# Performance work log

Hardware: AMD Instinct MI355X
Metric: run time of the kernel (lower is better)

## Reference

```python
import jax, jax.numpy as jnp
import numpy as np

EPS = 1e-8  # F.cosine_similarity default eps


def setup_inputs() -> dict:
    key = jax.random.key(0)
    k1, k2, k3 = jax.random.split(key, 3)
    C, S, Q, D_IN, Z_DIM = 256, 5, 64, 1024, 128
    xs = jax.random.normal(k1, (C, S, D_IN), dtype=jnp.float32)
    xq = jax.random.normal(k2, (C, Q, D_IN), dtype=jnp.float32)
    W = jax.random.normal(k3, (D_IN, Z_DIM), dtype=jnp.float32) / np.sqrt(D_IN)
    return {"xs": xs, "xq": xq, "W": W}


def _protonet_loss(xs, xq, W):
    C, S, D = xs.shape
    Q = xq.shape[1]
    # encoder (linear) applied to concatenated support+query, as in the original
    x = jnp.concatenate([xs.reshape(C * S, D), xq.reshape(C * Q, D)], axis=0)
    z = x @ W                                   # [C*(S+Q), Zd]
    Zd = z.shape[-1]
    z_proto = z[: C * S].reshape(C, S, Zd).mean(axis=1)   # [C, Zd]
    zq = z[C * S:]                                        # [C*Q, Zd]
    # squared euclidean distance (GEMM form, avoids [CQ, C, Zd] intermediate)
    d2 = (jnp.sum(zq * zq, axis=-1, keepdims=True)
          + jnp.sum(z_proto * z_proto, axis=-1)[None, :]
          - 2.0 * (zq @ z_proto.T))                       # [C*Q, C]
    lp = d2.reshape(C, Q, C)                              # label_predicts
    # leave-one-out: for each class i drop column i -> [C, Q, C-1]
    loo_idx = np.stack([np.delete(np.arange(C), i) for i in range(C)])  # [C, C-1]
    idx = jnp.broadcast_to(jnp.asarray(loo_idx)[:, None, :], (C, Q, C - 1))
    loo = jnp.take_along_axis(lp, idx, axis=2)            # [C, Q, C-1]
    # pairwise cosine similarity between query rows j<k, per class
    nrm = jnp.maximum(jnp.linalg.norm(loo, axis=-1), EPS)
    a = loo / nrm[..., None]
    sim = jnp.einsum('cqd,ckd->cqk', a, a)                # [C, Q, Q]
    pair_mask = jnp.triu(jnp.ones((Q, Q), dtype=bool), 1)
    n_pairs = C * (Q * (Q - 1) // 2)
    cos_loss = jnp.sum(jnp.where(pair_mask[None], sim, 0.0)) / n_pairs
    # log_softmax over prototype axis; accuracy vs diagonal targets
    log_p_y = jax.nn.log_softmax(-d2, axis=1).reshape(C, Q, C)
    y_hat = jnp.argmax(log_p_y, axis=2)                   # [C, Q]
    acc = jnp.mean((y_hat == jnp.arange(C)[:, None]).astype(jnp.float32))
    # original overwrites loss_val with the cosine-similarity loss
    return cos_loss, acc


def reference(xs, xq, W):
    return _protonet_loss(xs, xq, W)
```

## Files before the change

kernel.cpp:

```cpp
#include <hip/hip_runtime.h>


typedef __attribute__((ext_vector_type(8))) short s8v;
typedef __attribute__((ext_vector_type(4))) float f32x4;

__device__ __forceinline__ short f2bf(float f) {
  union { float f; unsigned u; } v; v.f = f;
  unsigned r = (v.u + 0x7fffu + ((v.u >> 16) & 1u)) >> 16;
  return (short)r;
}

__global__ void k_zero(float* __restrict__ out) {
  if (threadIdx.x < 2) out[threadIdx.x] = 0.0f;
}

__global__ void k_xbar(const float* __restrict__ xs, float* __restrict__ xbar) {
  const int c = blockIdx.x;
  const float* b = xs + (size_t)c * 5120;
  for (int e = threadIdx.x; e < 1024; e += 256) {
    float s = b[e] + b[1024 + e] + b[2048 + e] + b[3072 + e] + b[4096 + e];
    xbar[(size_t)c * 1024 + e] = s * 0.2f;
  }
}

__global__ __launch_bounds__(256) void k_wt(const float* __restrict__ W,
                                            unsigned short* __restrict__ Wt) {
  __shared__ unsigned short T[128 * 68];
  const int tid = threadIdx.x;
  const int kb = blockIdx.x * 64;
#pragma unroll
  for (int s = 0; s < 8; ++s) {
    int idx = tid + s * 256;
    int kr = idx >> 5, n4 = idx & 31;
    float4 v = *(const float4*)(W + (size_t)(kb + kr) * 128 + n4 * 4);
    T[(n4 * 4 + 0) * 68 + kr] = (unsigned short)f2bf(v.x);
    T[(n4 * 4 + 1) * 68 + kr] = (unsigned short)f2bf(v.y);
    T[(n4 * 4 + 2) * 68 + kr] = (unsigned short)f2bf(v.z);
    T[(n4 * 4 + 3) * 68 + kr] = (unsigned short)f2bf(v.w);
  }
  __syncthreads();
#pragma unroll
  for (int s = 0; s < 8; ++s) {
    int idx = tid + s * 256;
    int n = idx >> 4, k4 = idx & 15;
    ushort4 o;
    o.x = T[n * 68 + k4 * 4 + 0];
    o.y = T[n * 68 + k4 * 4 + 1];
    o.z = T[n * 68 + k4 * 4 + 2];
    o.w = T[n * 68 + k4 * 4 + 3];
    *(ushort4*)(Wt + (size_t)n * 1024 + kb + k4 * 4) = o;
  }
}

__global__ __launch_bounds__(64) void k_gemm_z(
    const float* __restrict__ xbar, const float* __restrict__ xq,
    const unsigned short* __restrict__ Wt,
    unsigned short* __restrict__ zb, float* __restrict__ n2) {
  const int rb = blockIdx.x * 16;
  const int lane = threadIdx.x & 63, ln = lane & 15, q = lane >> 4;
  const float* abase = (rb < 256) ? (xbar + (size_t)rb * 1024)
                                  : (xq + (size_t)(rb - 256) * 1024);
  const float* arow = abase + (size_t)ln * 1024 + q * 8;
  f32x4 acc[8] = {};
  float4 a0 = *(const float4*)(arow);
  float4 a1 = *(const float4*)(arow + 4);
  for (int kt = 0; kt < 32; ++kt) {
    float4 p0, p1;
    if (kt < 31) {
      p0 = *(const float4*)(arow + (kt + 1) * 32);
      p1 = *(const float4*)(arow + (kt + 1) * 32 + 4);
    }
    s8v af = { f2bf(a0.x), f2bf(a0.y), f2bf(a0.z), f2bf(a0.w),
               f2bf(a1.x), f2bf(a1.y), f2bf(a1.z), f2bf(a1.w) };
#pragma unroll
    for (int t = 0; t < 8; ++t) {
      s8v bf = *(const s8v*)(Wt + (size_t)(t * 16 + ln) * 1024 + kt * 32 + q * 8);
      acc[t] = __builtin_amdgcn_mfma_f32_16x16x32_bf16(af, bf, acc[t], 0, 0, 0);
    }
    a0 = p0; a1 = p1;
  }
#pragma unroll
  for (int p = 0; p < 4; ++p) {
    int grow = rb + q * 4 + p;
    float sp = 0.0f;
#pragma unroll
    for (int t = 0; t < 8; ++t) {
      float v = acc[t][p];
      zb[(size_t)grow * 128 + t * 16 + ln] = (unsigned short)f2bf(v);
      sp += v * v;
    }
    sp += __shfl_xor(sp, 1);
    sp += __shfl_xor(sp, 2);
    sp += __shfl_xor(sp, 4);
    sp += __shfl_xor(sp, 8);
    if (ln == 0) n2[grow] = sp;
  }
}

__global__ __launch_bounds__(256) void k_d2red(
    const unsigned short* __restrict__ zb, const float* __restrict__ n2,
    float* __restrict__ out) {
  __shared__ float Dt[256 * 65];
  __shared__ float rv[256];
  __shared__ int   ri[256];
  __shared__ float rss[256];
  __shared__ float invn[64];
  __shared__ float sred[4];
  __shared__ float s_tc, s_aq2, s_corr;
  const int tid = threadIdx.x;
  const int c = blockIdx.x;
  const int w = tid >> 6, lane = tid & 63, ln = lane & 15, qd = lane >> 4;

  f32x4 acc[16] = {};
  const unsigned short* Az = zb + (size_t)(256 + c * 64 + w * 16 + ln) * 128;
#pragma unroll
  for (int kt = 0; kt < 4; ++kt) {
    s8v af = *(const s8v*)(Az + kt * 32 + qd * 8);
#pragma unroll
    for (int t = 0; t < 16; ++t) {
      s8v bf = *(const s8v*)(zb + (size_t)(t * 16 + ln) * 128 + kt * 32 + qd * 8);
      acc[t] = __builtin_amdgcn_mfma_f32_16x16x32_bf16(af, bf, acc[t], 0, 0, 0);
    }
  }
#pragma unroll
  for (int p = 0; p < 4; ++p) {
    int qloc = w * 16 + qd * 4 + p;
    float qn = n2[256 + c * 64 + qloc];
#pragma unroll
    for (int t = 0; t < 16; ++t) {
      int j = t * 16 + ln;
      Dt[j * 65 + qloc] = qn + n2[j] - 2.0f * acc[t][p];
    }
  }
  __syncthreads();

  {
    const int q = tid & 63, jb = (tid >> 6) * 64;
    float mn = 3.4e38f; int mi = 0; float ss = 0.0f;
    for (int jj = 0; jj < 64; ++jj) {
      int j = jb + jj;
      float f = Dt[j * 65 + q];
      ss += f * f;
      if (f < mn) { mn = f; mi = j; }
    }
    rv[tid] = mn; ri[tid] = mi; rss[tid] = ss;
  }
  __syncthreads();
  if (tid < 64) {
    float bm = rv[tid]; int bi = ri[tid]; float ss = rss[tid];
    for (int h = 1; h < 4; ++h) {
      float v = rv[h * 64 + tid];
      ss += rss[h * 64 + tid];
      if (v < bm) { bm = v; bi = ri[h * 64 + tid]; }
    }
    float col = Dt[c * 65 + tid];
    float loo2 = fmaxf(ss - col * col, 0.0f);
    float nrm = fmaxf(sqrtf(loo2), 1e-8f);
    float inv = 1.0f / nrm;
    invn[tid] = inv;
    float aq2 = loo2 * inv * inv;
    float corr = (bi == c) ? 1.0f : 0.0f;
    for (int m = 1; m < 64; m <<= 1) {
      aq2 += __shfl_xor(aq2, m);
      corr += __shfl_xor(corr, m);
    }
    if (tid == 0) { s_aq2 = aq2; s_corr = corr; }
  }
  __syncthreads();
  float t = 0.0f;
  for (int qq = 0; qq < 64; ++qq) t += Dt[tid * 65 + qq] * invn[qq];
  if (tid == c) s_tc = t;
  float t2 = t * t;
  for (int m = 1; m < 64; m <<= 1) t2 += __shfl_xor(t2, m);
  if ((tid & 63) == 0) sred[tid >> 6] = t2;
  __syncthreads();
  if (tid == 0) {
    float S2 = sred[0] + sred[1] + sred[2] + sred[3];
    float bs = 0.5f * (S2 - s_tc * s_tc - s_aq2);
    atomicAdd(&out[0], bs * (1.0f / 516096.0f));
    atomicAdd(&out[1], s_corr * (1.0f / 16384.0f));
  }
}

extern "C" void kernel_launch(void* const* d_in, const int* in_sizes, int n_in,
                              void* d_out, int out_size, void* d_ws, size_t ws_size,
                              hipStream_t stream) {
  const float* xs = (const float*)d_in[0];
  const float* xq = (const float*)d_in[1];
  const float* W  = (const float*)d_in[2];
  float* out = (float*)d_out;

  float* ws = (float*)d_ws;
  float* xbar = ws;
  unsigned short* Wt = (unsigned short*)(xbar + 262144);
  unsigned short* zb = Wt + 131072;
  float* n2 = (float*)(zb + (size_t)16640 * 128);

  k_zero<<<dim3(1), dim3(64), 0, stream>>>(out);
  k_xbar<<<dim3(256), dim3(256), 0, stream>>>(xs, xbar);
  k_wt<<<dim3(16), dim3(256), 0, stream>>>(W, Wt);
  k_gemm_z<<<dim3(1040), dim3(64), 0, stream>>>(xbar, xq, Wt, zb, n2);
  k_d2red<<<dim3(256), dim3(256), 0, stream>>>(zb, n2, out);
}
```

Baseline: 160.7 us.

## Fuse prep kernels and double-buffer A/B fragment loads in projection GEMM

Merges the zeroing, support-mean and weight-transpose kernels into one launch, removing two kernel launches and their serialization gaps. The projection GEMM now prefetches the next k-step's W fragments and the A rows two steps ahead into register double buffers, with the k loop fully unrolled, so global load latency is hidden behind MFMAs. Launch bounds with a minimum of one block per CU are added to the GEMM and reduction kernels, which lets the compiler use more registers but may reduce occupancy.

```diff
diff --git a/kernel.cpp b/kernel.cpp
--- a/kernel.cpp
+++ b/kernel.cpp
@@ -10,49 +10,48 @@
   return (short)r;
 }
 
-__global__ void k_zero(float* __restrict__ out) {
-  if (threadIdx.x < 2) out[threadIdx.x] = 0.0f;
-}
-
-__global__ void k_xbar(const float* __restrict__ xs, float* __restrict__ xbar) {
-  const int c = blockIdx.x;
-  const float* b = xs + (size_t)c * 5120;
-  for (int e = threadIdx.x; e < 1024; e += 256) {
-    float s = b[e] + b[1024 + e] + b[2048 + e] + b[3072 + e] + b[4096 + e];
-    xbar[(size_t)c * 1024 + e] = s * 0.2f;
-  }
-}
-
-__global__ __launch_bounds__(256) void k_wt(const float* __restrict__ W,
-                                            unsigned short* __restrict__ Wt) {
+__global__ __launch_bounds__(256) void k_prep(
+    const float* __restrict__ xs, const float* __restrict__ W,
+    float* __restrict__ xbar, unsigned short* __restrict__ Wt,
+    float* __restrict__ out) {
   __shared__ unsigned short T[128 * 68];
   const int tid = threadIdx.x;
-  const int kb = blockIdx.x * 64;
-#pragma unroll
-  for (int s = 0; s < 8; ++s) {
-    int idx = tid + s * 256;
-    int kr = idx >> 5, n4 = idx & 31;
-    float4 v = *(const float4*)(W + (size_t)(kb + kr) * 128 + n4 * 4);
-    T[(n4 * 4 + 0) * 68 + kr] = (unsigned short)f2bf(v.x);
-    T[(n4 * 4 + 1) * 68 + kr] = (unsigned short)f2bf(v.y);
-    T[(n4 * 4 + 2) * 68 + kr] = (unsigned short)f2bf(v.z);
-    T[(n4 * 4 + 3) * 68 + kr] = (unsigned short)f2bf(v.w);
-  }
-  __syncthreads();
-#pragma unroll
-  for (int s = 0; s < 8; ++s) {
-    int idx = tid + s * 256;
-    int n = idx >> 4, k4 = idx & 15;
-    ushort4 o;
-    o.x = T[n * 68 + k4 * 4 + 0];
-    o.y = T[n * 68 + k4 * 4 + 1];
-    o.z = T[n * 68 + k4 * 4 + 2];
-    o.w = T[n * 68 + k4 * 4 + 3];
-    *(ushort4*)(Wt + (size_t)n * 1024 + kb + k4 * 4) = o;
-  }
-}
-
-__global__ __launch_bounds__(64) void k_gemm_z(
+  if (blockIdx.x < 256) {
+    const int c = blockIdx.x;
+    if (c == 0 && tid < 2) out[tid] = 0.0f;
+    const float* b = xs + (size_t)c * 5120;
+    for (int e = tid; e < 1024; e += 256) {
+      float s = b[e] + b[1024 + e] + b[2048 + e] + b[3072 + e] + b[4096 + e];
+      xbar[(size_t)c * 1024 + e] = s * 0.2f;
+    }
+  } else {
+    const int kb = (blockIdx.x - 256) * 64;
+#pragma unroll
+    for (int s = 0; s < 8; ++s) {
+      int idx = tid + s * 256;
+      int kr = idx >> 5, n4 = idx & 31;
+      float4 v = *(const float4*)(W + (size_t)(kb + kr) * 128 + n4 * 4);
+      T[(n4 * 4 + 0) * 68 + kr] = (unsigned short)f2bf(v.x);
+      T[(n4 * 4 + 1) * 68 + kr] = (unsigned short)f2bf(v.y);
+      T[(n4 * 4 + 2) * 68 + kr] = (unsigned short)f2bf(v.z);
+      T[(n4 * 4 + 3) * 68 + kr] = (unsigned short)f2bf(v.w);
+    }
+    __syncthreads();
+#pragma unroll
+    for (int s = 0; s < 8; ++s) {
+      int idx = tid + s * 256;
+      int n = idx >> 4, k4 = idx & 15;
+      ushort4 o;
+      o.x = T[n * 68 + k4 * 4 + 0];
+      o.y = T[n * 68 + k4 * 4 + 1];
+      o.z = T[n * 68 + k4 * 4 + 2];
+      o.w = T[n * 68 + k4 * 4 + 3];
+      *(ushort4*)(Wt + (size_t)n * 1024 + kb + k4 * 4) = o;
+    }
+  }
+}
+
+__global__ __launch_bounds__(64, 1) void k_gemm_z(
     const float* __restrict__ xbar, const float* __restrict__ xq,
     const unsigned short* __restrict__ Wt,
     unsigned short* __restrict__ zb, float* __restrict__ n2) {
@@ -61,23 +60,35 @@
   const float* abase = (rb < 256) ? (xbar + (size_t)rb * 1024)
                                   : (xq + (size_t)(rb - 256) * 1024);
   const float* arow = abase + (size_t)ln * 1024 + q * 8;
+  const unsigned short* brow = Wt + (size_t)ln * 1024 + q * 8;
   f32x4 acc[8] = {};
-  float4 a0 = *(const float4*)(arow);
-  float4 a1 = *(const float4*)(arow + 4);
+  float4 a0[2], a1[2];
+  s8v bfr[2][8];
+  a0[0] = *(const float4*)(arow + 0);
+  a1[0] = *(const float4*)(arow + 4);
+  a0[1] = *(const float4*)(arow + 32);
+  a1[1] = *(const float4*)(arow + 36);
+#pragma unroll
+  for (int t = 0; t < 8; ++t)
+    bfr[0][t] = *(const s8v*)(brow + (size_t)t * 16 * 1024);
+#pragma unroll
   for (int kt = 0; kt < 32; ++kt) {
-    float4 p0, p1;
+    const int cur = kt & 1;
     if (kt < 31) {
-      p0 = *(const float4*)(arow + (kt + 1) * 32);
-      p1 = *(const float4*)(arow + (kt + 1) * 32 + 4);
-    }
-    s8v af = { f2bf(a0.x), f2bf(a0.y), f2bf(a0.z), f2bf(a0.w),
-               f2bf(a1.x), f2bf(a1.y), f2bf(a1.z), f2bf(a1.w) };
-#pragma unroll
-    for (int t = 0; t < 8; ++t) {
-      s8v bf = *(const s8v*)(Wt + (size_t)(t * 16 + ln) * 1024 + kt * 32 + q * 8);
-      acc[t] = __builtin_amdgcn_mfma_f32_16x16x32_bf16(af, bf, acc[t], 0, 0, 0);
-    }
-    a0 = p0; a1 = p1;
+#pragma unroll
+      for (int t = 0; t < 8; ++t)
+        bfr[cur ^ 1][t] =
+            *(const s8v*)(brow + (size_t)t * 16 * 1024 + (kt + 1) * 32);
+    }
+    s8v af = { f2bf(a0[cur].x), f2bf(a0[cur].y), f2bf(a0[cur].z), f2bf(a0[cur].w),
+               f2bf(a1[cur].x), f2bf(a1[cur].y), f2bf(a1[cur].z), f2bf(a1[cur].w) };
+    if (kt < 30) {
+      a0[cur] = *(const float4*)(arow + (kt + 2) * 32);
+      a1[cur] = *(const float4*)(arow + (kt + 2) * 32 + 4);
+    }
+#pragma unroll
+    for (int t = 0; t < 8; ++t)
+      acc[t] = __builtin_amdgcn_mfma_f32_16x16x32_bf16(af, bfr[cur][t], acc[t], 0, 0, 0);
   }
 #pragma unroll
   for (int p = 0; p < 4; ++p) {
@@ -97,7 +108,7 @@
   }
 }
 
-__global__ __launch_bounds__(256) void k_d2red(
+__global__ __launch_bounds__(256, 1) void k_d2red(
     const unsigned short* __restrict__ zb, const float* __restrict__ n2,
     float* __restrict__ out) {
   __shared__ float Dt[256 * 65];
@@ -196,9 +207,7 @@
   unsigned short* zb = Wt + 131072;
   float* n2 = (float*)(zb + (size_t)16640 * 128);
 
-  k_zero<<<dim3(1), dim3(64), 0, stream>>>(out);
-  k_xbar<<<dim3(256), dim3(256), 0, stream>>>(xs, xbar);
-  k_wt<<<dim3(16), dim3(256), 0, stream>>>(W, Wt);
+  k_prep<<<dim3(272), dim3(256), 0, stream>>>(xs, W, xbar, Wt, out);
   k_gemm_z<<<dim3(1040), dim3(64), 0, stream>>>(xbar, xq, Wt, zb, n2);
   k_d2red<<<dim3(256), dim3(256), 0, stream>>>(zb, n2, out);
 }
```

New measurement: 152.8 us. 1.05x faster.
